# Optimization experiments

Hardware: AMD Instinct MI355X
Metric: run time of the kernel (lower is better)

The kernel has to match this reference:

```python
import jax, jax.numpy as jnp
import numpy as np

B, L, C, Y, DIM = 64, 64, 4, 0, 2  # batch, lattice size, n_colors, tau-shift, shift axis


def _coloring_probes():
    # k x k block coloring for C colors (C must be a perfect square here; C=4 -> k=2)
    k = int(round(np.sqrt(C)))
    i = np.arange(L)[:, None]
    j = np.arange(L)[None, :]
    col = (i % k) * k + (j % k)  # (L, L) color index per site
    probes = (col[None, :, :] == np.arange(C)[:, None, None]).astype(np.float32)
    return jnp.asarray(probes)  # (C, L, L) one-hot color masks


def _gelu(x):
    return jax.nn.gelu(x, approximate=False)  # torch nn.GELU default = exact erf


def _forward(x, sW1, sb1, sW2, sb2, sW3, sb3, aW1, ab1, aW2, ab2):
    # site features: phi, 2D lattice laplacian (periodic), phi_{x+tau}, phi_{x-tau}
    lap = (jnp.roll(x, 1, 1) + jnp.roll(x, -1, 1)
           + jnp.roll(x, 1, 2) + jnp.roll(x, -1, 2) - 4.0 * x)
    phi_tau = jnp.roll(x, -Y, axis=DIM)
    phi_mtau = jnp.roll(x, Y, axis=DIM)
    f = jnp.stack([x, lap, phi_tau, phi_mtau], axis=-1)  # (B, L, L, 4)
    h = _gelu(f @ sW1 + sb1)
    h = _gelu(h @ sW2 + sb2)
    h = (h @ sW3 + sb3)[..., 0]                          # (B, L, L)
    h_mean = h.mean(axis=(1, 2))
    h_var = jnp.var(h, axis=(1, 2), ddof=1)              # torch .var() is unbiased
    h_sq_mean = (h * h).mean(axis=(1, 2))
    a = jnp.stack([h_mean, h_var, h_sq_mean], axis=1)    # (B, 3)
    a = _gelu(a @ aW1 + ab1)
    return (a @ aW2 + ab2)[..., 0]                       # (B,)


def setup_inputs() -> dict:
    key = jax.random.key(0)
    ks = jax.random.split(key, 8)

    def w(k, shape, fan_in):
        return jax.random.normal(k, shape, jnp.float32) / np.sqrt(fan_in).astype(np.float32)

    return {
        "x": jax.random.normal(ks[0], (B, L, L), jnp.float32),
        "signs": jax.random.randint(ks[1], (C, B, L, L), 0, 2, jnp.int32),
        "site_W1": w(ks[2], (4, 128), 4),
        "site_b1": jnp.zeros((128,), jnp.float32),
        "site_W2": w(ks[3], (128, 128), 128),
        "site_b2": jnp.zeros((128,), jnp.float32),
        "site_W3": w(ks[4], (128, 1), 128),
        "site_b3": jnp.zeros((1,), jnp.float32),
        "agg_W1": w(ks[5], (3, 64), 3),
        "agg_b1": jnp.zeros((64,), jnp.float32),
        "agg_W2": w(ks[6], (64, 1), 64),
        "agg_b2": jnp.zeros((1,), jnp.float32),
    }


def reference(x, signs, site_W1, site_b1, site_W2, site_b2, site_W3, site_b3,
              agg_W1, agg_b1, agg_W2, agg_b2):
    params = (site_W1, site_b1, site_W2, site_b2, site_W3, site_b3,
              agg_W1, agg_b1, agg_W2, agg_b2)
    fsum = lambda xx: _forward(xx, *params).sum()  # batches are independent, so sum is safe

    # first-order gradient grad_x F, shape (B, L, L)
    grad = jax.grad(fsum)(x)

    # probing laplacian with coloring + Rademacher signs, batched over colors
    probes = _coloring_probes()                                   # (C, L, L)
    z = (2.0 * signs.astype(jnp.float32) - 1.0) * probes[:, None]  # (C, B, L, L)
    # hvp_c = H @ z_c via forward-over-reverse AD (replaces per-color autograd.grad loop)
    hvp = jax.vmap(lambda zc: jax.jvp(jax.grad(fsum), (x,), (zc,))[1])(z)  # (C, B, L, L)
    lapl = jnp.sum(hvp * z, axis=(0, 2, 3))                       # (B,)

    # pack (grad, lapl) into one array: (B, L*L + 1)
    return jnp.concatenate([grad.reshape(B, -1), lapl[:, None]], axis=1)
```

## Files before the change

kernel.cpp:

```cpp
#include <hip/hip_runtime.h>
#include <hip/hip_bf16.h>
#include <math.h>

typedef unsigned short ushort_t;
typedef unsigned int   u32;
typedef __attribute__((ext_vector_type(8))) short s8v;
typedef __attribute__((ext_vector_type(4))) float f4v;
typedef __attribute__((ext_vector_type(2))) float f2v;

#define LL 64
#define NB 64
#define NSITE 4096
#define BN 262144
#define RED_OFF 0
#define LP_OFF  10240
#define WA_OFF  11264
#define WB_OFF  11392
#define PL_OFF  12288
#define BF_OFF  (PL_OFF + 6*BN)

#if __has_builtin(__builtin_amdgcn_exp2f)
#define EXP2F(x) __builtin_amdgcn_exp2f(x)
#else
#define EXP2F(x) __expf(0.6931471805599453f*(x))
#endif

__device__ __forceinline__ void gelu3(float u, float &h, float &d, float &e){
  float E   = __expf(-0.5f * u * u);
  float phi = 0.3989422804014327f * E;
  float az  = fabsf(u) * 0.70710678118654752f;
  float t   = __builtin_amdgcn_rcpf(1.0f + 0.3275911f * az);
  float p   = t*(0.254829592f + t*(-0.284496736f + t*(1.421413741f + t*(-1.453152027f + t*1.061405429f))));
  float erfabs = 1.0f - p * E;
  float erfv   = __builtin_copysignf(erfabs, u);
  float Phi = 0.5f * (1.0f + erfv);
  h = u * Phi;
  d = Phi + u * phi;
  e = phi * (2.0f - u * u);
}

__device__ __forceinline__ void gelu3x2(f2v u, f2v &h, f2v &d, f2v &e){
  f2v u2 = u * u;
  f2v m  = u2 * (-0.72134752044448170368f);
  f2v E;  E.x = EXP2F(m.x); E.y = EXP2F(m.y);
  f2v phi = 0.3989422804014327f * E;
  f2v az;
  az.x = fabsf(u.x) * 0.70710678118654752f;
  az.y = fabsf(u.y) * 0.70710678118654752f;
  f2v den = 0.3275911f * az + 1.0f;
  f2v t;  t.x = __builtin_amdgcn_rcpf(den.x); t.y = __builtin_amdgcn_rcpf(den.y);
  f2v p = t*(0.254829592f + t*(-0.284496736f + t*(1.421413741f + t*(-1.453152027f + t*1.061405429f))));
  f2v erfabs = 1.0f - p * E;
  f2v erfv;
  erfv.x = __builtin_copysignf(erfabs.x, u.x);
  erfv.y = __builtin_copysignf(erfabs.y, u.y);
  f2v Phi = 0.5f * erfv + 0.5f;
  h = u * Phi;
  d = u * phi + Phi;
  e = phi * (2.0f - u2);
}

#define DPP_ADD(v, ctrl) { \
  int _si = __builtin_amdgcn_update_dpp(0, __builtin_bit_cast(int, v), ctrl, 0xf, 0xf, true); \
  v += __builtin_bit_cast(float, _si); }

__device__ __forceinline__ float redjb16(float v){
  DPP_ADD(v, 0xB1);
  DPP_ADD(v, 0x4E);
  DPP_ADD(v, 0x124);
  DPP_ADD(v, 0x128);
  return v;
}
__device__ __forceinline__ float red64(float v){
  v = redjb16(v);
  v += __shfl_xor(v, 16);
  v += __shfl_xor(v, 32);
  return v;
}

__device__ __forceinline__ float redpair(float a, float b, bool hi8){
  float t = hi8 ? b : a;
  float o = hi8 ? a : b;
  int _s = __builtin_amdgcn_update_dpp(0, __builtin_bit_cast(int, o), 0x128, 0xf, 0xf, true);
  t += __builtin_bit_cast(float, _s);
  DPP_ADD(t, 0xB1);
  DPP_ADD(t, 0x4E);
  DPP_ADD(t, 0x141);
  return t;
}

__device__ __forceinline__ ushort_t bf16rne(float v){
  union { float f; u32 i; } x; x.f = v;
  u32 r = x.i + 0x7FFFu + ((x.i >> 16) & 1u);
  return (ushort_t)(r >> 16);
}
__device__ __forceinline__ u32 pkbf(float a, float b){
  __hip_bfloat162 t = __float22bfloat162_rn(make_float2(a, b));
  u32 r;
  __builtin_memcpy(&r, &t, sizeof(r));
  return r;
}
__device__ __forceinline__ u32 pkbf2(f2v v){
  return pkbf(v.x, v.y);
}

__global__ __launch_bounds__(256, 4) void k_pre(
    const float* __restrict__ W1g, const float* __restrict__ W2g,
    float* __restrict__ ws)
{
  int t = blockIdx.x * 256 + threadIdx.x;
  if (blockIdx.x == 0 && threadIdx.x < 128) {
    int k = threadIdx.x;
    ws[WA_OFF + k] = W1g[k] + W1g[256+k] + W1g[384+k];
    ws[WB_OFF + k] = W1g[128+k];
  }
  short* BF = (short*)(ws + BF_OFF);
  int w = t >> 9, nt = (t >> 8) & 1, kt = (t >> 6) & 3, lane = t & 63;
  int q = lane >> 4, nlo = lane & 15;
  int n = w*32 + nt*16 + nlo;
  s8v vh;
  #pragma unroll
  for (int jj = 0; jj < 8; ++jj) {
    int k = kt*32 + q*8 + jj;
    vh[jj] = (short)bf16rne(W2g[k*128 + n]);
  }
  *(s8v*)&BF[t*8] = vh;
}

__global__ __launch_bounds__(256, 4) void k_c1(
    const float* __restrict__ xg, const int* __restrict__ signs,
    const float* __restrict__ b1g, const float* __restrict__ b2g,
    const float* __restrict__ W3g, const float* __restrict__ b3g,
    float* __restrict__ ws)
{
  __shared__ alignas(16) short AF[12288];
  __shared__ float xS[6][64];
  __shared__ char  zS[6][64];
  __shared__ float EP[16][7][4];

  const int tid  = threadIdx.x;
  const int lane = tid & 63;
  const int w    = tid >> 6;
  const int q    = lane >> 4;
  const int nlo  = lane & 15;
  const bool hi8 = (nlo & 8) != 0;

  const int blk = blockIdx.x;
  const int b   = blk >> 4;
  const int i0  = (blk & 15) << 2;

  const s8v* BhT = (const s8v*)((const short*)(ws + BF_OFF)) + (w*512 + lane);
  s8v Bfrag[8];
  #pragma unroll
  for (int kt = 0; kt < 4; ++kt) {
    Bfrag[kt]   = BhT[kt*64];
    Bfrag[4+kt] = BhT[256 + kt*64];
  }

  float b2j[2], w3j[2];
  #pragma unroll
  for (int nt = 0; nt < 2; ++nt) {
    int j = w*32 + nt*16 + nlo;
    b2j[nt] = b2g[j];
    w3j[nt] = W3g[j];
  }
  float b3v = b3g[0];
  const f2v b2p = {b2j[0], b2j[1]};
  const f2v w3p = {w3j[0], w3j[1]};

  const int s_  = tid & 15;
  const int ko_ = tid >> 4;
  float4 waH[2], wbH[2], b1H[2];
  #pragma unroll
  for (int half = 0; half < 2; ++half) {
    int k0 = ko_*8 + half*4;
    waH[half] = *(const float4*)(ws + WA_OFF + k0);
    wbH[half] = *(const float4*)(ws + WB_OFF + k0);
    b1H[half] = *(const float4*)(b1g + k0);
  }

  for (int t = tid; t < 384; t += 256) {
    int r = t >> 6, j = t & 63;
    int gr = (i0 - 1 + r) & 63;
    xS[r][j] = xg[(size_t)b*NSITE + gr*64 + j];
    int c = ((gr & 1) << 1) | (j & 1);
    zS[r][j] = (char)(2*signs[((c*NB + b)*LL + gr)*LL + j] - 1);
  }
  __syncthreads();

  float racc[10];
  #pragma unroll
  for (int n = 0; n < 10; ++n) racc[n] = 0.f;

  #pragma unroll 1
  for (int ch = 0; ch < 16; ++ch) {
    const int lr = 1 + (ch >> 2);
    const int jb = ch & 3;
    const int i  = i0 + (ch >> 2);

    {
      int j = jb*16 + s_, jm = (j+63)&63, jp = (j+1)&63;
      float p = xS[lr][j];
      float l = xS[lr-1][j] + xS[lr+1][j] + xS[lr][jm] + xS[lr][jp] - 4.0f*p;
      u32 vv[6][4];
      #pragma unroll
      for (int half = 0; half < 2; ++half) {
        const float* waA = (const float*)&waH[half];
        const float* wbA = (const float*)&wbH[half];
        const float* b1A = (const float*)&b1H[half];
        #pragma unroll
        for (int pr = 0; pr < 2; ++pr) {
          f2v wa = {waA[pr*2], waA[pr*2+1]};
          f2v wb = {wbA[pr*2], wbA[pr*2+1]};
          f2v bb = {b1A[pr*2], b1A[pr*2+1]};
          f2v u = p*wa + l*wb + bb;
          f2v h, dd, ee;
          gelu3x2(u, h, dd, ee);
          int c = half*2 + pr;
          vv[0][c] = pkbf2(h);
          vv[1][c] = pkbf2(dd*wa);
          vv[2][c] = pkbf2(dd*wb);
          f2v ea = ee*wa, eb = ee*wb;
          vv[3][c] = pkbf2(ea*wa);
          vv[4][c] = pkbf2(ea*wb);
          vv[5][c] = pkbf2(eb*wb);
        }
      }
      short* base = &AF[(ko_>>2)*3072 + ((ko_&3)*16 + s_)*8];
      #pragma unroll
      for (int pp = 0; pp < 6; ++pp)
        *(int4*)&base[pp*512] = make_int4((int)vv[pp][0], (int)vv[pp][1],
                                          (int)vv[pp][2], (int)vv[pp][3]);
    }
    __syncthreads();

    f4v acc[6][2];
    #pragma unroll
    for (int pp = 0; pp < 6; ++pp)
      #pragma unroll
      for (int nt = 0; nt < 2; ++nt)
        acc[pp][nt] = (f4v){0.f, 0.f, 0.f, 0.f};

    __builtin_amdgcn_s_setprio(1);
    #pragma unroll 1
    for (int kt = 0; kt < 4; ++kt) {
      const short* base = &AF[kt*3072 + lane*8];
      #pragma unroll
      for (int pp = 0; pp < 6; ++pp) {
        s8v ah = *(const s8v*)&base[pp*512];
        acc[pp][0] = __builtin_amdgcn_mfma_f32_16x16x32_bf16(ah, Bfrag[kt],   acc[pp][0], 0, 0, 0);
        acc[pp][1] = __builtin_amdgcn_mfma_f32_16x16x32_bf16(ah, Bfrag[4+kt], acc[pp][1], 0, 0, 0);
      }
    }
    __builtin_amdgcn_s_setprio(0);

    {
      #pragma unroll
      for (int r = 0; r < 4; ++r) {
        f2v uu = (f2v){acc[0][0][r], acc[0][1][r]} + b2p;
        f2v h2, d2, e2;
        gelu3x2(uu, h2, d2, e2);
        f2v wd = w3p*d2, we = w3p*e2;
        f2v A  = (f2v){acc[1][0][r], acc[1][1][r]};
        f2v Bv = (f2v){acc[2][0][r], acc[2][1][r]};
        f2v t3 = (f2v){acc[3][0][r], acc[3][1][r]};
        f2v t4 = (f2v){acc[4][0][r], acc[4][1][r]};
        f2v t5 = (f2v){acc[5][0][r], acc[5][1][r]};
        f2v vsh = w3p*h2;
        f2v vsA = wd*A;
        f2v vsB = wd*Bv;
        f2v vsa = we*(A*A)   + wd*t3;
        f2v vsb = we*(A*Bv)  + wd*t4;
        f2v vsc = we*(Bv*Bv) + wd*t5;
        float sh = vsh.x + vsh.y;
        float sA = vsA.x + vsA.y;
        float sB = vsB.x + vsB.y;
        float sa = vsa.x + vsa.y;
        float sb = vsb.x + vsb.y;
        float sc = vsc.x + vsc.y;
        float r01 = redpair(sh, sA, hi8);
        float r23 = redpair(sB, sa, hi8);
        float r45 = redpair(sb, sc, hi8);
        if ((nlo & 7) == 0) {
          int site = q*4 + r;
          int off = nlo >> 3;
          EP[site][0+off][w] = r01;
          EP[site][2+off][w] = r23;
          EP[site][4+off][w] = r45;
        }
      }
    }
    __syncthreads();

    if (tid < 16) {
      int s = tid;
      float h = 0.f, RA = 0.f, RB = 0.f, TAa = 0.f, TAb = 0.f, TBb = 0.f;
      #pragma unroll
      for (int ww = 0; ww < 4; ++ww) {
        h   += EP[s][0][ww];
        RA  += EP[s][1][ww];
        RB  += EP[s][2][ww];
        TAa += EP[s][3][ww];
        TAb += EP[s][4][ww];
        TBb += EP[s][5][ww];
      }
      h += b3v;
      float* P = ws + PL_OFF;
      int j = jb*16 + s;
      size_t site = (size_t)b*NSITE + i*64 + j;
      P[0*BN + site] = h;
      P[1*BN + site] = RA;
      P[2*BN + site] = RB;
      P[3*BN + site] = TAa;
      P[4*BN + site] = TAb;
      P[5*BN + site] = TBb;

      int jm = (j+63)&63, jp = (j+1)&63;
      int c0 = ((i & 1) << 1) | (j & 1);
      float hd[4] = {0.f, 0.f, 0.f, 0.f};
      hd[c0]     = (float)zS[lr][j] * (RA - 4.0f*RB);
      hd[c0 ^ 1] = (float)(zS[lr][jm] + zS[lr][jp]) * RB;
      hd[c0 ^ 2] = (float)(zS[lr-1][j] + zS[lr+1][j]) * RB;
      racc[0] += h;
      racc[1] += h*h;
      #pragma unroll
      for (int cc = 0; cc < 4; ++cc) {
        racc[2+cc] += hd[cc];
        racc[6+cc] += h*hd[cc];
      }
    }
  }

  if (tid < 16) {
    #pragma unroll
    for (int n = 0; n < 10; ++n) racc[n] = redjb16(racc[n]);
    if (tid == 0) {
      #pragma unroll
      for (int n = 0; n < 10; ++n) ws[RED_OFF + blk*10 + n] = racc[n];
    }
  }
}

__global__ __launch_bounds__(256, 1) void k_c2(
    const int* __restrict__ signs,
    const float* __restrict__ aW1g, const float* __restrict__ ab1g,
    const float* __restrict__ aW2g,
    float* __restrict__ ws, float* __restrict__ out)
{
  __shared__ float part[4];
  __shared__ float coefL[10];
  __shared__ float redS[10];
  __shared__ float cbS[6][64];
  int blk = blockIdx.x;
  int b = blk >> 4, rg = blk & 15;
  int tid = threadIdx.x;

  if (tid < 160) {
    int qq = tid >> 4, g = tid & 15;
    float v = ws[RED_OFF + (b*16 + g)*10 + qq];
    v = redjb16(v);
    if (g == 0) redS[qq] = v;
  }
  __syncthreads();

  if (tid < 64) {
    int k = tid;
    const float Nf = 4096.0f, Nm1 = 4095.0f;
    float S1 = redS[0], S2 = redS[1];
    float m = S1/Nf, q = S2/Nf;
    float v = (S2 - S1*S1/Nf)/Nm1;
    float w0 = aW1g[k], w1 = aW1g[64+k], w2 = aW1g[128+k];
    float t = m*w0 + v*w1 + q*w2 + ab1g[k];
    float gh, gd, ge;
    gelu3(t, gh, gd, ge);
    float o = aW2g[k];
    float g1o = gd*o, g2o = ge*o;
    float da0 = w0*g1o, da1 = w1*g1o, da2 = w2*g1o;
    float M00 = w0*w0*g2o, M01 = w0*w1*g2o, M02 = w0*w2*g2o;
    float M11 = w1*w1*g2o, M12 = w1*w2*g2o, M22 = w2*w2*g2o;
    da0 = red64(da0); da1 = red64(da1); da2 = red64(da2);
    M00 = red64(M00); M01 = red64(M01); M02 = red64(M02);
    M11 = red64(M11); M12 = red64(M12); M22 = red64(M22);
    if (k == 0) {
      coefL[0] = da0/Nf - 2.0f*da1*m/Nm1;
      coefL[1] = 2.0f*da1/Nm1 + 2.0f*da2/Nf;
      #pragma unroll
      for (int c = 0; c < 4; ++c) {
        float s1 = redS[2 + c], s2 = redS[6 + c];
        float md = s1/Nf, qd = 2.0f*s2/Nf;
        float vd = (2.0f*s2 - 2.0f*S1*s1/Nf)/Nm1;
        float dd0 = M00*md + M01*vd + M02*qd;
        float dd1 = M01*md + M11*vd + M12*qd;
        float dd2 = M02*md + M12*vd + M22*qd;
        coefL[2+c] = dd0/Nf - 2.0f*(dd1*m + da1*md)/Nm1;
        coefL[6+c] = 2.0f*dd1/Nm1 + 2.0f*dd2/Nf;
      }
    }
  }
  __syncthreads();

  const float* P = ws + PL_OFF;
  int base = b*NSITE;
  float alpha = coefL[0], beta = coefL[1];

  for (int t = tid; t < 384; t += 256) {
    int r = t >> 6, jj = t & 63;
    int gr = (rg*4 - 1 + r) & 63;
    int sidx = base + gr*64 + jj;
    cbS[r][jj] = (alpha + beta*P[sidx]) * P[2*BN + sidx];
  }
  __syncthreads();

  int rl = tid >> 6, j = tid & 63;
  int i = rg*4 + rl;
  int im=(i+63)&63, ip=(i+1)&63, jm=(j+63)&63, jp=(j+1)&63;
  int s  = base + i*64 + j;
  float h  = P[s], RA = P[BN+s], RB = P[2*BN+s];
  float TAa= P[3*BN+s], TAb = P[4*BN+s], TBb = P[5*BN+s];
  float g  = alpha + beta*h;
  int lr2 = rl + 1;
  float cb  = cbS[lr2][j];
  float cbu = cbS[lr2-1][j], cbd = cbS[lr2+1][j];
  float cbl = cbS[lr2][jm],  cbr = cbS[lr2][jp];
  float grad = g*RA + (cbu + cbd + cbl + cbr - 4.0f*cb);
  out[(size_t)b*4097 + i*64 + j] = grad;

  int c0 = ((i & 1) << 1) | (j & 1);
  int c1 = c0 ^ 1, c2 = c0 ^ 2;
  float zv = 2.0f*(float)signs[((c0*NB + b)*LL + i )*LL + j ] - 1.0f;
  float zl = 2.0f*(float)signs[((c1*NB + b)*LL + i )*LL + jm] - 1.0f;
  float zr = 2.0f*(float)signs[((c1*NB + b)*LL + i )*LL + jp] - 1.0f;
  float zu = 2.0f*(float)signs[((c2*NB + b)*LL + im)*LL + j ] - 1.0f;
  float zd = 2.0f*(float)signs[((c2*NB + b)*LL + ip)*LL + j ] - 1.0f;
  float sjr = zl + zr, sud = zu + zd;
  float hd0 = zv*(RA - 4.0f*RB);
  float hd1 = sjr*RB, hd2 = sud*RB;
  float gd0 = coefL[2+c0] + coefL[6+c0]*h + beta*hd0;
  float gd1 = coefL[2+c1] + coefL[6+c1]*h + beta*hd1;
  float gd2 = coefL[2+c2] + coefL[6+c2]*h + beta*hd2;
  float ca0 = gd0*RA + g*( zv*TAa - 4.0f*zv*TAb );
  float cb0 = gd0*RB + g*( zv*TAb - 4.0f*zv*TBb );
  float cb1 = gd1*RB + g*( sjr*TBb );
  float cb2 = gd2*RB + g*( sud*TBb );
  float contrib = zv*ca0 - 4.0f*zv*cb0 + sjr*cb1 + sud*cb2;

  float vsum = red64(contrib);
  int wv = tid >> 6;
  if ((tid & 63) == 0) part[wv] = vsum;
  __syncthreads();
  if (tid == 0)
    ws[LP_OFF + blk] = part[0] + part[1] + part[2] + part[3];
}

__global__ void k_e(const float* __restrict__ ws, float* __restrict__ out){
  int b = threadIdx.x;
  if (b < 64) {
    float s = 0.f;
    #pragma unroll
    for (int g = 0; g < 16; ++g) s += ws[LP_OFF + b*16 + g];
    out[(size_t)b*4097 + 4096] = s;
  }
}

extern "C" void kernel_launch(void* const* d_in, const int* in_sizes, int n_in,
                              void* d_out, int out_size, void* d_ws, size_t ws_size,
                              hipStream_t stream) {
  const float* xg    = (const float*)d_in[0];
  const int*   signs = (const int*)d_in[1];
  const float* W1    = (const float*)d_in[2];
  const float* b1    = (const float*)d_in[3];
  const float* W2    = (const float*)d_in[4];
  const float* b2    = (const float*)d_in[5];
  const float* W3    = (const float*)d_in[6];
  const float* b3    = (const float*)d_in[7];
  const float* aW1   = (const float*)d_in[8];
  const float* ab1   = (const float*)d_in[9];
  const float* aW2   = (const float*)d_in[10];
  float* ws  = (float*)d_ws;
  float* out = (float*)d_out;

  hipLaunchKernelGGL(k_pre, dim3(8),    dim3(256), 0, stream, W1, W2, ws);
  hipLaunchKernelGGL(k_c1,  dim3(1024), dim3(256), 0, stream,
                     xg, signs, b1, b2, W3, b3, ws);
  hipLaunchKernelGGL(k_c2,  dim3(1024), dim3(256), 0, stream,
                     signs, aW1, ab1, aW2, ws, out);
  hipLaunchKernelGGL(k_e,   dim3(1),    dim3(64),  0, stream, ws, out);
}
```

Baseline: 208.8 us.

## Split k_c1 work across 512 threads with one N-tile per wave

```diff
diff --git a/kernel.cpp b/kernel.cpp
--- a/kernel.cpp
+++ b/kernel.cpp
@@ -127,7 +127,7 @@
   *(s8v*)&BF[t*8] = vh;
 }
 
-__global__ __launch_bounds__(256, 4) void k_c1(
+__global__ __launch_bounds__(512, 6) void k_c1(
     const float* __restrict__ xg, const int* __restrict__ signs,
     const float* __restrict__ b1g, const float* __restrict__ b2g,
     const float* __restrict__ W3g, const float* __restrict__ b3g,
@@ -136,7 +136,7 @@
   __shared__ alignas(16) short AF[12288];
   __shared__ float xS[6][64];
   __shared__ char  zS[6][64];
-  __shared__ float EP[16][7][4];
+  __shared__ float EP[16][7][8];
 
   const int tid  = threadIdx.x;
   const int lane = tid & 63;
@@ -149,38 +149,23 @@
   const int b   = blk >> 4;
   const int i0  = (blk & 15) << 2;
 
-  const s8v* BhT = (const s8v*)((const short*)(ws + BF_OFF)) + (w*512 + lane);
-  s8v Bfrag[8];
-  #pragma unroll
-  for (int kt = 0; kt < 4; ++kt) {
-    Bfrag[kt]   = BhT[kt*64];
-    Bfrag[4+kt] = BhT[256 + kt*64];
-  }
-
-  float b2j[2], w3j[2];
-  #pragma unroll
-  for (int nt = 0; nt < 2; ++nt) {
-    int j = w*32 + nt*16 + nlo;
-    b2j[nt] = b2g[j];
-    w3j[nt] = W3g[j];
-  }
-  float b3v = b3g[0];
-  const f2v b2p = {b2j[0], b2j[1]};
-  const f2v w3p = {w3j[0], w3j[1]};
+  const s8v* Bh = (const s8v*)((const short*)(ws + BF_OFF))
+                  + ((w >> 1)*512 + (w & 1)*256 + lane);
+
+  const int n_  = w*16 + nlo;
+  const float b2s = b2g[n_];
+  const float w3s = W3g[n_];
+  const float b3v = b3g[0];
 
   const int s_  = tid & 15;
-  const int ko_ = tid >> 4;
-  float4 waH[2], wbH[2], b1H[2];
-  #pragma unroll
-  for (int half = 0; half < 2; ++half) {
-    int k0 = ko_*8 + half*4;
-    waH[half] = *(const float4*)(ws + WA_OFF + k0);
-    wbH[half] = *(const float4*)(ws + WB_OFF + k0);
-    b1H[half] = *(const float4*)(b1g + k0);
-  }
-
-  for (int t = tid; t < 384; t += 256) {
-    int r = t >> 6, j = t & 63;
+  const int kq_ = tid >> 4;
+  short* afb = &AF[(kq_ >> 3)*3072 + (((kq_ & 7) >> 1)*16 + s_)*8 + (kq_ & 1)*4];
+  const float4 waQ = *(const float4*)(ws + WA_OFF + kq_*4);
+  const float4 wbQ = *(const float4*)(ws + WB_OFF + kq_*4);
+  const float4 b1Q = *(const float4*)(b1g + kq_*4);
+
+  if (tid < 384) {
+    int r = tid >> 6, j = tid & 63;
     int gr = (i0 - 1 + r) & 63;
     xS[r][j] = xg[(size_t)b*NSITE + gr*64 + j];
     int c = ((gr & 1) << 1) | (j & 1);
@@ -202,91 +187,81 @@
       int j = jb*16 + s_, jm = (j+63)&63, jp = (j+1)&63;
       float p = xS[lr][j];
       float l = xS[lr-1][j] + xS[lr+1][j] + xS[lr][jm] + xS[lr][jp] - 4.0f*p;
-      u32 vv[6][4];
-      #pragma unroll
-      for (int half = 0; half < 2; ++half) {
-        const float* waA = (const float*)&waH[half];
-        const float* wbA = (const float*)&wbH[half];
-        const float* b1A = (const float*)&b1H[half];
-        #pragma unroll
-        for (int pr = 0; pr < 2; ++pr) {
-          f2v wa = {waA[pr*2], waA[pr*2+1]};
-          f2v wb = {wbA[pr*2], wbA[pr*2+1]};
-          f2v bb = {b1A[pr*2], b1A[pr*2+1]};
-          f2v u = p*wa + l*wb + bb;
-          f2v h, dd, ee;
-          gelu3x2(u, h, dd, ee);
-          int c = half*2 + pr;
-          vv[0][c] = pkbf2(h);
-          vv[1][c] = pkbf2(dd*wa);
-          vv[2][c] = pkbf2(dd*wb);
-          f2v ea = ee*wa, eb = ee*wb;
-          vv[3][c] = pkbf2(ea*wa);
-          vv[4][c] = pkbf2(ea*wb);
-          vv[5][c] = pkbf2(eb*wb);
-        }
-      }
-      short* base = &AF[(ko_>>2)*3072 + ((ko_&3)*16 + s_)*8];
+      const float* waA = (const float*)&waQ;
+      const float* wbA = (const float*)&wbQ;
+      const float* b1A = (const float*)&b1Q;
+      u32 vv[6][2];
+      #pragma unroll
+      for (int pr = 0; pr < 2; ++pr) {
+        f2v wa = {waA[pr*2], waA[pr*2+1]};
+        f2v wb = {wbA[pr*2], wbA[pr*2+1]};
+        f2v bb = {b1A[pr*2], b1A[pr*2+1]};
+        f2v u = p*wa + l*wb + bb;
+        f2v h, dd, ee;
+        gelu3x2(u, h, dd, ee);
+        vv[0][pr] = pkbf2(h);
+        vv[1][pr] = pkbf2(dd*wa);
+        vv[2][pr] = pkbf2(dd*wb);
+        f2v ea = ee*wa, eb = ee*wb;
+        vv[3][pr] = pkbf2(ea*wa);
+        vv[4][pr] = pkbf2(ea*wb);
+        vv[5][pr] = pkbf2(eb*wb);
+      }
       #pragma unroll
       for (int pp = 0; pp < 6; ++pp)
-        *(int4*)&base[pp*512] = make_int4((int)vv[pp][0], (int)vv[pp][1],
-                                          (int)vv[pp][2], (int)vv[pp][3]);
+        *(int2*)&afb[pp*512] = make_int2((int)vv[pp][0], (int)vv[pp][1]);
     }
     __syncthreads();
 
-    f4v acc[6][2];
+    f4v acc[6];
     #pragma unroll
     for (int pp = 0; pp < 6; ++pp)
-      #pragma unroll
-      for (int nt = 0; nt < 2; ++nt)
-        acc[pp][nt] = (f4v){0.f, 0.f, 0.f, 0.f};
+      acc[pp] = (f4v){0.f, 0.f, 0.f, 0.f};
 
     __builtin_amdgcn_s_setprio(1);
     #pragma unroll 1
     for (int kt = 0; kt < 4; ++kt) {
+      s8v bh = Bh[kt*64];
       const short* base = &AF[kt*3072 + lane*8];
       #pragma unroll
       for (int pp = 0; pp < 6; ++pp) {
         s8v ah = *(const s8v*)&base[pp*512];
-        acc[pp][0] = __builtin_amdgcn_mfma_f32_16x16x32_bf16(ah, Bfrag[kt],   acc[pp][0], 0, 0, 0);
-        acc[pp][1] = __builtin_amdgcn_mfma_f32_16x16x32_bf16(ah, Bfrag[4+kt], acc[pp][1], 0, 0, 0);
+        acc[pp] = __builtin_amdgcn_mfma_f32_16x16x32_bf16(ah, bh, acc[pp], 0, 0, 0);
       }
     }
     __builtin_amdgcn_s_setprio(0);
 
     {
       #pragma unroll
-      for (int r = 0; r < 4; ++r) {
-        f2v uu = (f2v){acc[0][0][r], acc[0][1][r]} + b2p;
+      for (int pr = 0; pr < 2; ++pr) {
+        const int r0 = pr*2;
+        f2v uu = (f2v){acc[0][r0], acc[0][r0+1]} + b2s;
         f2v h2, d2, e2;
         gelu3x2(uu, h2, d2, e2);
-        f2v wd = w3p*d2, we = w3p*e2;
-        f2v A  = (f2v){acc[1][0][r], acc[1][1][r]};
-        f2v Bv = (f2v){acc[2][0][r], acc[2][1][r]};
-        f2v t3 = (f2v){acc[3][0][r], acc[3][1][r]};
-        f2v t4 = (f2v){acc[4][0][r], acc[4][1][r]};
-        f2v t5 = (f2v){acc[5][0][r], acc[5][1][r]};
-        f2v vsh = w3p*h2;
+        f2v wd = w3s*d2, we = w3s*e2;
+        f2v A  = (f2v){acc[1][r0], acc[1][r0+1]};
+        f2v Bv = (f2v){acc[2][r0], acc[2][r0+1]};
+        f2v t3 = (f2v){acc[3][r0], acc[3][r0+1]};
+        f2v t4 = (f2v){acc[4][r0], acc[4][r0+1]};
+        f2v t5 = (f2v){acc[5][r0], acc[5][r0+1]};
+        f2v vsh = w3s*h2;
         f2v vsA = wd*A;
         f2v vsB = wd*Bv;
         f2v vsa = we*(A*A)   + wd*t3;
         f2v vsb = we*(A*Bv)  + wd*t4;
         f2v vsc = we*(Bv*Bv) + wd*t5;
-        float sh = vsh.x + vsh.y;
-        float sA = vsA.x + vsA.y;
-        float sB = vsB.x + vsB.y;
-        float sa = vsa.x + vsa.y;
-        float sb = vsb.x + vsb.y;
-        float sc = vsc.x + vsc.y;
-        float r01 = redpair(sh, sA, hi8);
-        float r23 = redpair(sB, sa, hi8);
-        float r45 = redpair(sb, sc, hi8);
-        if ((nlo & 7) == 0) {
-          int site = q*4 + r;
-          int off = nlo >> 3;
-          EP[site][0+off][w] = r01;
-          EP[site][2+off][w] = r23;
-          EP[site][4+off][w] = r45;
+        #pragma unroll
+        for (int rr = 0; rr < 2; ++rr) {
+          float r01 = redpair(vsh[rr], vsA[rr], hi8);
+          float r23 = redpair(vsB[rr], vsa[rr], hi8);
+          float r45 = redpair(vsb[rr], vsc[rr], hi8);
+          if ((nlo & 7) == 0) {
+            int site = q*4 + r0 + rr;
+            int off = nlo >> 3;
+            EP[site][0+off][w] = r01;
+            EP[site][2+off][w] = r23;
+            EP[site][4+off][w] = r45;
+          }
         }
       }
     }
@@ -296,7 +271,7 @@
       int s = tid;
       float h = 0.f, RA = 0.f, RB = 0.f, TAa = 0.f, TAb = 0.f, TBb = 0.f;
       #pragma unroll
-      for (int ww = 0; ww < 4; ++ww) {
+      for (int ww = 0; ww < 8; ++ww) {
         h   += EP[s][0][ww];
         RA  += EP[s][1][ww];
         RB  += EP[s][2][ww];
@@ -480,7 +455,7 @@
   float* out = (float*)d_out;
 
   hipLaunchKernelGGL(k_pre, dim3(8),    dim3(256), 0, stream, W1, W2, ws);
-  hipLaunchKernelGGL(k_c1,  dim3(1024), dim3(256), 0, stream,
+  hipLaunchKernelGGL(k_c1,  dim3(1024), dim3(512), 0, stream,
                      xg, signs, b1, b2, W3, b3, ws);
   hipLaunchKernelGGL(k_c2,  dim3(1024), dim3(256), 0, stream,
                      signs, aW1, ab1, aW2, ws, out);
```

New measurement: 203.1 us. 2.7% less time.
